# Performance work log

Hardware: AMD Instinct MI355X
Metric: run time of the kernel (lower is better)

The kernel has to match this reference:

```python
import jax, jax.numpy as jnp
import numpy as np

BATCH, LENGTH, DIM = 8, 65536, 128
MAX_N_PEAKS = 512


def setup_inputs() -> dict:
    rng = np.random.default_rng(0)
    # per-sample number of peaks (each sample also has one trailing dropped chunk)
    n_peaks = rng.integers(400, MAX_N_PEAKS + 1, size=BATCH)
    chunk_sizes = []
    for i in range(BATCH):
        # n_peaks[i] cut points -> n_peaks[i]+1 chunks summing exactly to LENGTH
        cuts = np.sort(rng.choice(np.arange(1, LENGTH), size=int(n_peaks[i]), replace=False))
        sizes = np.diff(np.concatenate([[0], cuts, [LENGTH]]))
        chunk_sizes.append(sizes)
    chunk_size = np.concatenate(chunk_sizes).astype(np.int32)
    key = jax.random.key(0)
    x = jax.random.normal(key, (BATCH, LENGTH, DIM), dtype=jnp.float32)
    return {
        "x": x,
        "chunk_size": jnp.asarray(chunk_size),
        "n_peaks": jnp.asarray(n_peaks, dtype=jnp.int32),
        "max_n_peaks": MAX_N_PEAKS,
    }


def reference(x, chunk_size, n_peaks, max_n_peaks):
    # x: (B, L, D); chunk_size: (total_chunks,) summing to B*L;
    # n_peaks: (B,); sample i owns chunks [pool_start[i], pool_start[i]+n_peaks[i]+1),
    # the last chunk of each sample is dropped (matches pool_end = pool_idx - 1).
    batch, length, dim = x.shape
    total_chunks = chunk_size.shape[0]  # static
    x_flat = x.reshape(-1, dim)  # (B*L, D)

    # one fused segment-mean over all chunks
    seg_ids = jnp.repeat(jnp.arange(total_chunks), chunk_size,
                         total_repeat_length=batch * length)
    sums = jax.ops.segment_sum(x_flat, seg_ids, num_segments=total_chunks)
    counts = jnp.maximum(chunk_size, 1).astype(x.dtype)  # empty chunk -> zeros
    means = sums / counts[:, None]  # (total_chunks, D)

    # map chunk -> (sample, peak slot), scatter into padded output
    chunks_per_sample = n_peaks + 1
    pool_start = jnp.concatenate(
        [jnp.zeros((1,), n_peaks.dtype), jnp.cumsum(chunks_per_sample)[:-1]])
    sample_of_chunk = jnp.repeat(jnp.arange(batch), chunks_per_sample,
                                 total_repeat_length=total_chunks)
    peak_pos = jnp.arange(total_chunks) - pool_start[sample_of_chunk]
    valid = peak_pos < n_peaks[sample_of_chunk]  # drops trailing chunk per sample
    dest = jnp.where(valid, peak_pos, max_n_peaks)  # invalid -> scratch row
    out = jnp.zeros((batch, max_n_peaks + 1, dim), x.dtype)
    out = out.at[sample_of_chunk, dest].set(means)
    return out[:, :max_n_peaks]  # (B, max_n_peaks, D), zero-padded
```

## Files before the change

### kernel.cpp

```cpp
#include <hip/hip_runtime.h>
#include <hip/hip_bf16.h>


#define SCAN_THREADS 256

__global__ __launch_bounds__(SCAN_THREADS) void scan_kernel(
    const int* __restrict__ chunk_size, const int* __restrict__ n_peaks,
    int total_chunks, int batch,
    int* __restrict__ chunk_start, int* __restrict__ pool_start) {
  __shared__ int partials[SCAN_THREADS];
  const int t = threadIdx.x;
  const int items = (total_chunks + SCAN_THREADS - 1) / SCAN_THREADS;
  const int begin = t * items;
  const int end = min(begin + items, total_chunks);

  int local = 0;
  for (int i = begin; i < end; ++i) local += chunk_size[i];
  partials[t] = local;
  __syncthreads();

  for (int off = 1; off < SCAN_THREADS; off <<= 1) {
    int v = (t >= off) ? partials[t - off] : 0;
    __syncthreads();
    partials[t] += v;
    __syncthreads();
  }

  int run = (t == 0) ? 0 : partials[t - 1];
  for (int i = begin; i < end; ++i) {
    chunk_start[i] = run;
    run += chunk_size[i];
  }

  if (t == 0) {
    int acc = 0;
    for (int i = 0; i < batch; ++i) {
      pool_start[i] = acc;
      acc += n_peaks[i] + 1;
    }
  }
}

__global__ __launch_bounds__(256) void pool_kernel(
    const float* __restrict__ x, const int* __restrict__ chunk_size,
    const int* __restrict__ n_peaks, const int* __restrict__ chunk_start,
    const int* __restrict__ pool_start, float* __restrict__ out,
    int max_n_peaks) {
  const int b = blockIdx.x;
  const int i = b / max_n_peaks;
  const int p = b % max_n_peaks;
  const int t = threadIdx.x;
  const int dim4 = t & 31;
  const int r0 = t >> 5;

  const int np = n_peaks[i];
  float4 acc = make_float4(0.f, 0.f, 0.f, 0.f);
  int cnt = 1;

  if (p < np) {
    const int c = pool_start[i] + p;
    const int start = chunk_start[c];
    const int size = chunk_size[c];
    cnt = size > 0 ? size : 1;
    const float4* __restrict__ xp = (const float4*)x + (size_t)start * 32;
    for (int r = r0; r < size; r += 8) {
      float4 v = xp[(size_t)r * 32 + dim4];
      acc.x += v.x; acc.y += v.y; acc.z += v.z; acc.w += v.w;
    }
  }

  __shared__ float4 red[256];
  red[t] = acc;
  __syncthreads();

  if (t < 32) {
    float4 s = red[t];
#pragma unroll
    for (int k = 1; k < 8; ++k) {
      float4 v = red[t + 32 * k];
      s.x += v.x; s.y += v.y; s.z += v.z; s.w += v.w;
    }
    const float inv = (p < np) ? (1.0f / (float)cnt) : 0.0f;
    float4 m = make_float4(s.x * inv, s.y * inv, s.z * inv, s.w * inv);
    ((float4*)out)[(size_t)b * 32 + t] = m;
  }
}

extern "C" void kernel_launch(void* const* d_in, const int* in_sizes, int n_in,
                              void* d_out, int out_size, void* d_ws, size_t ws_size,
                              hipStream_t stream) {
  const float* x = (const float*)d_in[0];
  const int* chunk_size = (const int*)d_in[1];
  const int* n_peaks = (const int*)d_in[2];
  const int total_chunks = in_sizes[1];
  const int batch = in_sizes[2];
  const int dim = 128;
  const int max_n_peaks = out_size / (batch * dim);
  float* out = (float*)d_out;

  int* chunk_start = (int*)d_ws;
  int* pool_start = chunk_start + total_chunks;

  scan_kernel<<<1, SCAN_THREADS, 0, stream>>>(chunk_size, n_peaks, total_chunks,
                                              batch, chunk_start, pool_start);

  const int grid = batch * max_n_peaks;
  pool_kernel<<<grid, 256, 0, stream>>>(x, chunk_size, n_peaks, chunk_start,
                                        pool_start, out, max_n_peaks);
}
```

Baseline: 411.9 us.

## Split each chunk's reduction across four blocks and combine in a second kernel

Each chunk's row range is now divided among four blocks that write partial sums to workspace, and a separate combine kernel adds the partials, divides by the count and scatters into the padded output. This spreads the long, irregular per-chunk reductions over more blocks so load balance and memory-level parallelism improve. It also adds unroll-by-4 on the load loop. The cost is an extra kernel launch, a workspace round trip, and reductions over the dropped trailing chunks that the output never uses.

```diff
diff --git a/kernel.cpp b/kernel.cpp
--- a/kernel.cpp
+++ b/kernel.cpp
@@ -3,6 +3,7 @@
 
 
 #define SCAN_THREADS 256
+#define NSPLIT 4
 
 __global__ __launch_bounds__(SCAN_THREADS) void scan_kernel(
     const int* __restrict__ chunk_size, const int* __restrict__ n_peaks,
@@ -41,32 +42,27 @@
   }
 }
 
-__global__ __launch_bounds__(256) void pool_kernel(
+__global__ __launch_bounds__(256) void split_sum_kernel(
     const float* __restrict__ x, const int* __restrict__ chunk_size,
-    const int* __restrict__ n_peaks, const int* __restrict__ chunk_start,
-    const int* __restrict__ pool_start, float* __restrict__ out,
-    int max_n_peaks) {
-  const int b = blockIdx.x;
-  const int i = b / max_n_peaks;
-  const int p = b % max_n_peaks;
+    const int* __restrict__ chunk_start, float4* __restrict__ split_sums) {
+  const int c = blockIdx.x >> 2;
+  const int s = blockIdx.x & 3;
   const int t = threadIdx.x;
   const int dim4 = t & 31;
   const int r0 = t >> 5;
 
-  const int np = n_peaks[i];
+  const int start = chunk_start[c];
+  const int size = chunk_size[c];
+  const int rps = (size + NSPLIT - 1) >> 2;
+  const int r_begin = s * rps;
+  const int r_end = min(r_begin + rps, size);
+
+  const float4* __restrict__ xp = (const float4*)x + (size_t)start * 32;
   float4 acc = make_float4(0.f, 0.f, 0.f, 0.f);
-  int cnt = 1;
-
-  if (p < np) {
-    const int c = pool_start[i] + p;
-    const int start = chunk_start[c];
-    const int size = chunk_size[c];
-    cnt = size > 0 ? size : 1;
-    const float4* __restrict__ xp = (const float4*)x + (size_t)start * 32;
-    for (int r = r0; r < size; r += 8) {
-      float4 v = xp[(size_t)r * 32 + dim4];
-      acc.x += v.x; acc.y += v.y; acc.z += v.z; acc.w += v.w;
-    }
+#pragma unroll 4
+  for (int r = r_begin + r0; r < r_end; r += 8) {
+    float4 v = xp[(size_t)r * 32 + dim4];
+    acc.x += v.x; acc.y += v.y; acc.z += v.z; acc.w += v.w;
   }
 
   __shared__ float4 red[256];
@@ -74,16 +70,41 @@
   __syncthreads();
 
   if (t < 32) {
-    float4 s = red[t];
+    float4 sum = red[t];
 #pragma unroll
     for (int k = 1; k < 8; ++k) {
       float4 v = red[t + 32 * k];
-      s.x += v.x; s.y += v.y; s.z += v.z; s.w += v.w;
+      sum.x += v.x; sum.y += v.y; sum.z += v.z; sum.w += v.w;
     }
-    const float inv = (p < np) ? (1.0f / (float)cnt) : 0.0f;
-    float4 m = make_float4(s.x * inv, s.y * inv, s.z * inv, s.w * inv);
-    ((float4*)out)[(size_t)b * 32 + t] = m;
+    split_sums[((size_t)blockIdx.x) * 32 + t] = sum;
   }
+}
+
+__global__ __launch_bounds__(256) void combine_kernel(
+    const float4* __restrict__ split_sums, const int* __restrict__ chunk_size,
+    const int* __restrict__ n_peaks, const int* __restrict__ pool_start,
+    float4* __restrict__ out, int max_n_peaks, int n_slots) {
+  const int t = threadIdx.x;
+  const int slot = blockIdx.x * 8 + (t >> 5);
+  const int dim4 = t & 31;
+  if (slot >= n_slots) return;
+  const int i = slot / max_n_peaks;
+  const int p = slot % max_n_peaks;
+
+  float4 m = make_float4(0.f, 0.f, 0.f, 0.f);
+  if (p < n_peaks[i]) {
+    const int c = pool_start[i] + p;
+    float4 sum = make_float4(0.f, 0.f, 0.f, 0.f);
+#pragma unroll
+    for (int k = 0; k < NSPLIT; ++k) {
+      float4 v = split_sums[((size_t)c * NSPLIT + k) * 32 + dim4];
+      sum.x += v.x; sum.y += v.y; sum.z += v.z; sum.w += v.w;
+    }
+    const int sz = chunk_size[c];
+    const float inv = 1.0f / (float)(sz > 0 ? sz : 1);
+    m = make_float4(sum.x * inv, sum.y * inv, sum.z * inv, sum.w * inv);
+  }
+  out[(size_t)slot * 32 + dim4] = m;
 }
 
 extern "C" void kernel_launch(void* const* d_in, const int* in_sizes, int n_in,
@@ -100,11 +121,17 @@
 
   int* chunk_start = (int*)d_ws;
   int* pool_start = chunk_start + total_chunks;
+  size_t off = ((size_t)(total_chunks + batch) * sizeof(int) + 15) & ~(size_t)15;
+  float4* split_sums = (float4*)((char*)d_ws + off);
 
   scan_kernel<<<1, SCAN_THREADS, 0, stream>>>(chunk_size, n_peaks, total_chunks,
                                               batch, chunk_start, pool_start);
 
-  const int grid = batch * max_n_peaks;
-  pool_kernel<<<grid, 256, 0, stream>>>(x, chunk_size, n_peaks, chunk_start,
-                                        pool_start, out, max_n_peaks);
+  split_sum_kernel<<<total_chunks * NSPLIT, 256, 0, stream>>>(
+      x, chunk_size, chunk_start, split_sums);
+
+  const int n_slots = batch * max_n_peaks;
+  combine_kernel<<<(n_slots + 7) / 8, 256, 0, stream>>>(
+      split_sums, chunk_size, n_peaks, pool_start, (float4*)out, max_n_peaks,
+      n_slots);
 }
```

Result: faster. 369.7 us (-10.2%).
